# Performance work log

Hardware: AMD Instinct MI355X
Metric: run time of the kernel (lower is better)

## Reference

```python
import jax, jax.numpy as jnp
import numpy as np

B, S, C_IN, D, H = 16, 1024, 1280, 512, 8
HD = D // H  # head dim = 64
EPS = 1e-5


def _rope(x):
    # x: [b, h, s, d]; half-split rotation as in the torch module
    d = x.shape[-1]
    half = d // 2
    s = x.shape[2]
    inv_freq = 1.0 / (10000.0 ** (jnp.arange(0, d, 2, dtype=jnp.float32) / d))  # [half]
    ang = jnp.arange(s, dtype=jnp.float32)[:, None] * inv_freq[None, :]  # [s, half]
    sin, cos = jnp.sin(ang), jnp.cos(ang)  # broadcast over [b, h]
    x1, x2 = x[..., :half], x[..., half:]
    return jnp.concatenate([x1 * cos - x2 * sin, x1 * sin + x2 * cos], axis=-1)


def _ln(x, g, b):
    mu = jnp.mean(x, axis=-1, keepdims=True)
    var = jnp.mean((x - mu) ** 2, axis=-1, keepdims=True)
    return (x - mu) * jax.lax.rsqrt(var + EPS) * g + b


def setup_inputs() -> dict:
    key = jax.random.key(0)
    ks = jax.random.split(key, 12)
    def lin(k, fan_in, fan_out):
        lim = 1.0 / np.sqrt(fan_in)
        return jax.random.uniform(k, (fan_in, fan_out), jnp.float32, -lim, lim)
    return {
        "x": jax.random.normal(ks[0], (B, S, C_IN), jnp.float32),
        "w_in": lin(ks[1], C_IN, D), "b_in": jnp.zeros((D,), jnp.float32),
        "w_qkv": lin(ks[2], D, 3 * D), "b_qkv": jnp.zeros((3 * D,), jnp.float32),
        "w_out": lin(ks[3], D, D), "b_out": jnp.zeros((D,), jnp.float32),
        "w_ffn1": lin(ks[4], D, 4 * D), "b_ffn1": jnp.zeros((4 * D,), jnp.float32),
        "w_ffn2": lin(ks[5], 4 * D, D), "b_ffn2": jnp.zeros((D,), jnp.float32),
        "g1": jnp.ones((D,), jnp.float32), "bn1": jnp.zeros((D,), jnp.float32),
        "g2": jnp.ones((D,), jnp.float32), "bn2": jnp.zeros((D,), jnp.float32),
    }


def reference(x, w_in, b_in, w_qkv, b_qkv, w_out, b_out,
              w_ffn1, b_ffn1, w_ffn2, b_ffn2, g1, bn1, g2, bn2):
    h = x @ w_in + b_in  # [b, s, D]
    qkv = (h @ w_qkv + b_qkv).reshape(B, S, 3, H, HD)
    q, k, v = (jnp.transpose(qkv[:, :, i], (0, 2, 1, 3)) for i in range(3))  # [b, h, s, d]
    q, k = _rope(q), _rope(k)
    scores = jnp.einsum('bhqd,bhkd->bhqk', q, k) / np.sqrt(HD)
    attn = jax.nn.softmax(scores, axis=-1)
    o = jnp.einsum('bhqk,bhkd->bhqd', attn, v)
    o = jnp.transpose(o, (0, 2, 1, 3)).reshape(B, S, D)
    o = o @ w_out + b_out
    h = _ln(h + o, g1, bn1)
    ffn = jax.nn.relu(h @ w_ffn1 + b_ffn1) @ w_ffn2 + b_ffn2
    return _ln(h + ffn, g2, bn2)
```

## Files before the change

kernel.cpp:

```cpp
#include <hip/hip_runtime.h>
#include <hip/hip_bf16.h>
#include <math.h>

#define B_   16
#define S_   1024
#define CIN  1280
#define D_   512
#define H_   8
#define HD_  64
#define NROW (B_ * S_)

typedef __bf16 bf16;
typedef float  f32x2  __attribute__((ext_vector_type(2)));
typedef float  f32x4  __attribute__((ext_vector_type(4)));
typedef bf16   bf16x4 __attribute__((ext_vector_type(4)));
typedef bf16   bf16x8 __attribute__((ext_vector_type(8)));

__device__ __forceinline__ void gload_lds16(const bf16* g, bf16* l) {
    __builtin_amdgcn_global_load_lds(
        (const __attribute__((address_space(1))) void*)g,
        (__attribute__((address_space(3))) void*)l, 16, 0, 0);
}

#define SBAR()   __builtin_amdgcn_s_barrier()
#define SCHED0() __builtin_amdgcn_sched_barrier(0)
#define VMCNT8() asm volatile("s_waitcnt vmcnt(8)" ::: "memory")
#define VMCNT2() asm volatile("s_waitcnt vmcnt(2)" ::: "memory")
#define VMCNT0() asm volatile("s_waitcnt vmcnt(0)" ::: "memory")

__global__ void cvt_kernel(const float* __restrict__ in, bf16* __restrict__ out, int n4)
{
    int i = blockIdx.x * blockDim.x + threadIdx.x;
    if (i >= n4) return;
    f32x4 v = *(const f32x4*)(in + (size_t)i * 4);
    bf16x4 o;
    o[0] = (bf16)v[0]; o[1] = (bf16)v[1]; o[2] = (bf16)v[2]; o[3] = (bf16)v[3];
    *(bf16x4*)(out + (size_t)i * 4) = o;
}

__global__ __launch_bounds__(256)
void tr_cvt_kernel(const float* __restrict__ in, bf16* __restrict__ out, int R, int C)
{
    __shared__ float T[32][33];
    const int r0 = blockIdx.y << 5, c0 = blockIdx.x << 5;
    const int t  = threadIdx.x;
    {
        int lr = t >> 3, lc = (t & 7) << 2;
        f32x4 v = *(const f32x4*)(in + (size_t)(r0 + lr) * C + c0 + lc);
        T[lr][lc] = v[0]; T[lr][lc + 1] = v[1]; T[lr][lc + 2] = v[2]; T[lr][lc + 3] = v[3];
    }
    __syncthreads();
    {
        int oc = t >> 3, orr = (t & 7) << 2;
        bf16x4 o;
        o[0] = (bf16)T[orr][oc];     o[1] = (bf16)T[orr + 1][oc];
        o[2] = (bf16)T[orr + 2][oc]; o[3] = (bf16)T[orr + 3][oc];
        *(bf16x4*)(out + (size_t)(c0 + oc) * R + r0 + orr) = o;
    }
}

__global__ void cs_kernel(float* __restrict__ cs)
{
    int idx = blockIdx.x * 256 + threadIdx.x;
    int s = idx >> 5, i = idx & 31;
    float freq = exp2f(-(float)i * (13.287712379549449f / 32.f));
    float sn, c;
    sincosf((float)s * freq, &sn, &c);
    cs[(size_t)idx * 2]     = c;
    cs[(size_t)idx * 2 + 1] = sn;
}

#define ASZ1 (128 * 64)

template<int EPI, bool RELU, bool RES, bool OUTF, bool OUTB>
__global__ __launch_bounds__(256, 2)
void gemm128_kernel(const bf16* __restrict__ A, const bf16* __restrict__ Wt,
                    const float* __restrict__ bias, const bf16* __restrict__ res,
                    float* __restrict__ outf, bf16* __restrict__ outb,
                    const float* __restrict__ cs, bf16* __restrict__ vt,
                    int M, int N, int K)
{
    __shared__ bf16 lds[4 * ASZ1];

    const int tid  = threadIdx.x;
    const int lane = tid & 63;
    const int wid  = tid >> 6;

    const int perX = (M >> 7) >> 3;
    const int lin  = blockIdx.x;
    const int idx  = lin >> 3;
    const int my   = (lin & 7) * perX + (idx & (perX - 1));
    const int nx   = idx / perX;
    const int m0   = my << 7, n0 = nx << 7;

    const int sRow = lane >> 3;
    const int sK   = ((lane & 7) ^ sRow) << 3;

    const int r2  = wid >> 1;
    const int c2  = wid & 1;
    const int cc  = lane & 15;
    const int g   = (lane >> 4) & 3;
    const int swz = (cc & 7) << 4;

    f32x4 acc[4][4] = {};

    auto stage = [&](int t, int b) {
        const bf16* gA = A  + (size_t)m0 * K + t * 64;
        const bf16* gB = Wt + (size_t)n0 * K + t * 64;
        bf16* lA = lds + b * ASZ1;
        bf16* lB = lds + 2 * ASZ1 + b * ASZ1;
        #pragma unroll
        for (int v = 0; v < 4; ++v) {
            const int ch = v * 4 + wid;
            gload_lds16(gA + (size_t)(ch * 8 + sRow) * K + sK, lA + ch * 512);
            gload_lds16(gB + (size_t)(ch * 8 + sRow) * K + sK, lB + ch * 512);
        }
    };

    const int T = K >> 6;
    stage(0, 0);
    stage(1, 1);
    VMCNT8();
    SCHED0();
    SBAR();

    for (int t = 0; t < T; ++t) {
        const int b = t & 1;
        const char* lA = (const char*)(lds + b * ASZ1);
        const char* lB = (const char*)(lds + 2 * ASZ1 + b * ASZ1);

        #pragma unroll
        for (int ks = 0; ks < 2; ++ks) {
            bf16x8 af[4], bfr[4];
            #pragma unroll
            for (int i = 0; i < 4; ++i) {
                const int row = r2 * 64 + i * 16 + cc;
                af[i] = *(const bf16x8*)(lA + row * 128 + ((ks * 64 + g * 16) ^ swz));
            }
            #pragma unroll
            for (int j = 0; j < 4; ++j) {
                const int row = c2 * 64 + j * 16 + cc;
                bfr[j] = *(const bf16x8*)(lB + row * 128 + ((ks * 64 + g * 16) ^ swz));
            }
            __builtin_amdgcn_s_setprio(1);
            #pragma unroll
            for (int i = 0; i < 4; ++i)
                #pragma unroll
                for (int j = 0; j < 4; ++j)
                    acc[i][j] = __builtin_amdgcn_mfma_f32_16x16x32_bf16(af[i], bfr[j], acc[i][j], 0, 0, 0);
            __builtin_amdgcn_s_setprio(0);
        }
        SCHED0();
        SBAR();
        if (t + 2 < T) {
            stage(t + 2, b);
            VMCNT8();
        } else if (t + 1 < T) {
            VMCNT0();
        }
        if (t + 1 < T) { SCHED0(); SBAR(); }
    }

    const int rq = g << 2;
    if constexpr (EPI == 1) {
        const int colb = c2 * 64;
        if (nx < 8) {
            float bj[4];
            #pragma unroll
            for (int j = 0; j < 4; ++j) bj[j] = bias[n0 + colb + j * 16 + cc];
            #pragma unroll
            for (int i = 0; i < 4; ++i) {
                #pragma unroll
                for (int r = 0; r < 4; ++r) {
                    const int gm = m0 + r2 * 64 + i * 16 + rq + r;
                    const int s  = gm & (S_ - 1);
                    #pragma unroll
                    for (int jp = 0; jp < 2; ++jp) {
                        const int d = jp * 16 + cc;
                        f32x2 csv = *(const f32x2*)(cs + ((size_t)s * 32 + d) * 2);
                        float x1 = acc[i][jp][r]     + bj[jp];
                        float x2 = acc[i][jp + 2][r] + bj[jp + 2];
                        const size_t o1 = (size_t)gm * N + n0 + colb + d;
                        outb[o1]      = (bf16)(x1 * csv[0] - x2 * csv[1]);
                        outb[o1 + 32] = (bf16)(x1 * csv[1] + x2 * csv[0]);
                    }
                }
            }
        } else {
            const int col0 = n0 + colb;
            const int hw = (col0 >> 6) & 7;
            const int bb = m0 >> 10;
            bf16* vbase = vt + (size_t)(bb * 8 + hw) * (HD_ * S_);
            const int sb0 = (m0 & (S_ - 1)) + r2 * 64 + rq;
            #pragma unroll
            for (int i = 0; i < 4; ++i) {
                #pragma unroll
                for (int j = 0; j < 4; ++j) {
                    const int d = j * 16 + cc;
                    const float bv = bias[col0 + d];
                    bf16x4 pk;
                    #pragma unroll
                    for (int r = 0; r < 4; ++r) pk[r] = (bf16)(acc[i][j][r] + bv);
                    *(bf16x4*)(vbase + (size_t)d * S_ + sb0 + i * 16) = pk;
                }
            }
        }
    } else {
        #pragma unroll
        for (int i = 0; i < 4; ++i) {
            #pragma unroll
            for (int j = 0; j < 4; ++j) {
                const int gn = n0 + c2 * 64 + j * 16 + cc;
                const float bv = bias[gn];
                #pragma unroll
                for (int r = 0; r < 4; ++r) {
                    const int gm = m0 + r2 * 64 + i * 16 + rq + r;
                    float v = acc[i][j][r] + bv;
                    if (RES)  v += (float)res[(size_t)gm * N + gn];
                    if (RELU) v = fmaxf(v, 0.f);
                    if (OUTF) outf[(size_t)gm * N + gn] = v;
                    if (OUTB) outb[(size_t)gm * N + gn] = (bf16)v;
                }
            }
        }
    }
    (void)cs; (void)vt;
}

#define PST 72

__global__ __launch_bounds__(512)
void attn_kernel(const bf16* __restrict__ qkv, const bf16* __restrict__ vtg,
                 bf16* __restrict__ o)
{
    __shared__ bf16 Ks[2][4096];
    __shared__ bf16 Vs[2][4096];
    __shared__ bf16 Ps[8][16 * PST];

    const int bh  = blockIdx.x;
    const int b   = bh >> 3;
    const int h   = bh & 7;
    const int q0  = blockIdx.y << 7;
    const int tid = threadIdx.x;
    const int lane = tid & 63;
    const int w    = tid >> 6;
    const int c    = lane & 15;
    const int g    = lane >> 4;
    const int swz  = (c & 7) << 4;

    const size_t rs = 3 * D_;
    const bf16* qb = qkv + (size_t)b * S_ * rs + h * HD_;
    const bf16* kb = qb + D_;
    const bf16* vt = vtg + (size_t)bh * HD_ * S_;

    const int sRow = tid >> 3;
    const int sOff = ((tid & 7) ^ (sRow & 7)) << 3;

    bf16x8 qf[2];
    {
        const bf16* qrow = qb + (size_t)(q0 + w * 16 + c) * rs + g * 8;
        qf[0] = *(const bf16x8*)(qrow);
        qf[1] = *(const bf16x8*)(qrow + 32);
    }
    SCHED0();

    bf16x8 vones;
    {
        bf16 one = (bf16)(c == 0 ? 1.f : 0.f);
        #pragma unroll
        for (int u = 0; u < 8; ++u) vones[u] = one;
    }

    auto stage = [&](int t, int buf) {
        gload_lds16(kb + (size_t)(t * 64 + sRow) * rs + sOff, &Ks[buf][0] + (size_t)tid * 8);
        gload_lds16(vt + (size_t)sRow * S_ + t * 64 + sOff,   &Vs[buf][0] + (size_t)tid * 8);
    };

    f32x4 oa[4] = {};
    f32x4 oa5 = {};
    float m_r = -3.0e38f;
    const float CE  = 0.18033688011112042f;
    const float THR = 44.3614195558365f;

    stage(0, 0);
    stage(1, 1);
    VMCNT2();
    SCHED0();
    SBAR();

    for (int t = 0; t < 16; ++t) {
        const int buf = t & 1;
        const char* kB = (const char*)Ks[buf];
        const char* vB = (const char*)Vs[buf];

        f32x4 sa[4] = {};
        __builtin_amdgcn_s_setprio(1);
        #pragma unroll
        for (int ch = 0; ch < 2; ++ch)
            #pragma unroll
            for (int ks = 0; ks < 4; ++ks) {
                bf16x8 kf = *(const bf16x8*)(kB + (ks * 16 + c) * 128 + ((ch * 64 + g * 16) ^ swz));
                sa[ks] = __builtin_amdgcn_mfma_f32_16x16x32_bf16(kf, qf[ch], sa[ks], 0, 0, 0);
            }
        __builtin_amdgcn_s_setprio(0);

        float pmax = -3.0e38f;
        #pragma unroll
        for (int ks = 0; ks < 4; ++ks)
            pmax = fmaxf(pmax, fmaxf(fmaxf(sa[ks][0], sa[ks][1]), fmaxf(sa[ks][2], sa[ks][3])));
        pmax = fmaxf(pmax, __shfl_xor(pmax, 16, 64));
        pmax = fmaxf(pmax, __shfl_xor(pmax, 32, 64));

        if (!__all(pmax - m_r <= THR)) {
            float mnew = fmaxf(m_r, pmax);
            float sc = __builtin_amdgcn_exp2f((m_r - mnew) * CE);
            #pragma unroll
            for (int r = 0; r < 4; ++r) {
                float scr = __shfl(sc, g * 4 + r, 64);
                #pragma unroll
                for (int j = 0; j < 4; ++j) oa[j][r] *= scr;
                oa5[r] *= scr;
            }
            m_r = mnew;
        }

        const float nmCE = -m_r * CE;
        #pragma unroll
        for (int ks = 0; ks < 4; ++ks) {
            bf16x4 pb;
            #pragma unroll
            for (int r = 0; r < 4; ++r)
                pb[r] = (bf16)__builtin_amdgcn_exp2f(__builtin_fmaf(sa[ks][r], CE, nmCE));
            *(bf16x4*)&Ps[w][c * PST + ks * 16 + g * 4] = pb;
        }

        __builtin_amdgcn_s_setprio(1);
        #pragma unroll
        for (int ch = 0; ch < 2; ++ch) {
            bf16x8 pa = *(const bf16x8*)&Ps[w][c * PST + ch * 32 + g * 8];
            #pragma unroll
            for (int j = 0; j < 4; ++j) {
                bf16x8 vf = *(const bf16x8*)(vB + (j * 16 + c) * 128 + ((ch * 64 + g * 16) ^ swz));
                oa[j] = __builtin_amdgcn_mfma_f32_16x16x32_bf16(pa, vf, oa[j], 0, 0, 0);
            }
            oa5 = __builtin_amdgcn_mfma_f32_16x16x32_bf16(pa, vones, oa5, 0, 0, 0);
        }
        __builtin_amdgcn_s_setprio(0);

        SCHED0();
        SBAR();
        if (t + 2 < 16) {
            stage(t + 2, buf);
            VMCNT2();
        } else if (t + 1 < 16) {
            VMCNT0();
        }
        if (t + 1 < 16) { SCHED0(); SBAR(); }
    }

    float linv[4];
    #pragma unroll
    for (int r = 0; r < 4; ++r)
        linv[r] = 1.f / __shfl(oa5[r], lane & 48, 64);
    #pragma unroll
    for (int j = 0; j < 4; ++j)
        #pragma unroll
        for (int r = 0; r < 4; ++r) {
            int q = q0 + w * 16 + g * 4 + r;
            o[((size_t)(b * S_) + q) * D_ + h * HD_ + j * 16 + c] = (bf16)(oa[j][r] * linv[r]);
        }
}

template<bool OUTF, bool OUTB>
__global__ __launch_bounds__(256)
void ln_kernel(const float* __restrict__ in, const float* __restrict__ g,
               const float* __restrict__ be, float* __restrict__ outf,
               bf16* __restrict__ outb)
{
    const int row  = (blockIdx.x << 2) + (threadIdx.x >> 6);
    const int lane = threadIdx.x & 63;
    const float* p = in + (size_t)row * D_;
    f32x4 a  = *(const f32x4*)(p + lane * 4);
    f32x4 b2 = *(const f32x4*)(p + 256 + lane * 4);
    float s  = a[0] + a[1] + a[2] + a[3] + b2[0] + b2[1] + b2[2] + b2[3];
    float s2 = a[0]*a[0] + a[1]*a[1] + a[2]*a[2] + a[3]*a[3]
             + b2[0]*b2[0] + b2[1]*b2[1] + b2[2]*b2[2] + b2[3]*b2[3];
    #pragma unroll
    for (int off = 32; off; off >>= 1) {
        s  += __shfl_xor(s,  off, 64);
        s2 += __shfl_xor(s2, off, 64);
    }
    const float mean = s * (1.f / 512.f);
    const float var  = s2 * (1.f / 512.f) - mean * mean;
    const float rstd = rsqrtf(var + 1e-5f);

    f32x4 g0 = *(const f32x4*)(g + lane * 4);
    f32x4 g1 = *(const f32x4*)(g + 256 + lane * 4);
    f32x4 e0 = *(const f32x4*)(be + lane * 4);
    f32x4 e1 = *(const f32x4*)(be + 256 + lane * 4);
    f32x4 o0, o1;
    #pragma unroll
    for (int u = 0; u < 4; u++) {
        o0[u] = (a[u]  - mean) * rstd * g0[u] + e0[u];
        o1[u] = (b2[u] - mean) * rstd * g1[u] + e1[u];
    }
    if (OUTF) {
        float* of = outf + (size_t)row * D_;
        *(f32x4*)(of + lane * 4)       = o0;
        *(f32x4*)(of + 256 + lane * 4) = o1;
    }
    if (OUTB) {
        bf16x4 c0, c1;
        #pragma unroll
        for (int u = 0; u < 4; u++) { c0[u] = (bf16)o0[u]; c1[u] = (bf16)o1[u]; }
        bf16* ob = outb + (size_t)row * D_;
        *(bf16x4*)(ob + lane * 4)       = c0;
        *(bf16x4*)(ob + 256 + lane * 4) = c1;
    }
}

extern "C" void kernel_launch(void* const* d_in, const int* in_sizes, int n_in,
                              void* d_out, int out_size, void* d_ws, size_t ws_size,
                              hipStream_t stream)
{
    const float* x      = (const float*)d_in[0];
    const float* w_in   = (const float*)d_in[1];
    const float* b_in   = (const float*)d_in[2];
    const float* w_qkv  = (const float*)d_in[3];
    const float* b_qkv  = (const float*)d_in[4];
    const float* w_out  = (const float*)d_in[5];
    const float* b_out  = (const float*)d_in[6];
    const float* w_ffn1 = (const float*)d_in[7];
    const float* b_ffn1 = (const float*)d_in[8];
    const float* w_ffn2 = (const float*)d_in[9];
    const float* b_ffn2 = (const float*)d_in[10];
    const float* g1     = (const float*)d_in[11];
    const float* bn1    = (const float*)d_in[12];
    const float* g2     = (const float*)d_in[13];
    const float* bn2    = (const float*)d_in[14];

    char* ws = (char*)d_ws;
    constexpr size_t OFF_XB   = 0;
    constexpr size_t OFF_WIN  = OFF_XB   + 41943040ull;
    constexpr size_t OFF_WQKV = OFF_WIN  + 1310720ull;
    constexpr size_t OFF_WOUT = OFF_WQKV + 1572864ull;
    constexpr size_t OFF_WF1  = OFF_WOUT + 524288ull;
    constexpr size_t OFF_WF2  = OFF_WF1  + 2097152ull;
    constexpr size_t OFF_CS   = OFF_WF2  + 2097152ull;
    constexpr size_t OFF_HB   = OFF_CS   + 33554432ull;
    constexpr size_t OFF_QKV  = OFF_HB   + 16777216ull;
    constexpr size_t OFF_OB   = OFF_QKV  + 50331648ull;
    constexpr size_t OFF_VT   = OFF_OB   + 16777216ull;
    constexpr size_t OFF_H2B  = OFF_VT   + 33554432ull;
    constexpr size_t OFF_F1   = OFF_H2B  + 16777216ull;
    constexpr size_t OFF_T1   = OFF_XB;
    constexpr size_t OFF_T2   = OFF_QKV;

    bf16*  x_b    = (bf16*)(ws + OFF_XB);
    bf16*  win_t  = (bf16*)(ws + OFF_WIN);
    bf16*  wqkv_t = (bf16*)(ws + OFF_WQKV);
    bf16*  wout_t = (bf16*)(ws + OFF_WOUT);
    bf16*  wf1_t  = (bf16*)(ws + OFF_WF1);
    bf16*  wf2_t  = (bf16*)(ws + OFF_WF2);
    float* cs_t   = (float*)(ws + OFF_CS);
    bf16*  h_b    = (bf16*)(ws + OFF_HB);
    bf16*  qkv_b  = (bf16*)(ws + OFF_QKV);
    bf16*  o_b    = (bf16*)(ws + OFF_OB);
    bf16*  vt_g   = (bf16*)(ws + OFF_VT);
    bf16*  h2_b   = (bf16*)(ws + OFF_H2B);
    bf16*  f1_b   = (bf16*)(ws + OFF_F1);
    float* t1_f   = (float*)(ws + OFF_T1);
    float* t2_f   = (float*)(ws + OFF_T2);

    {
        int n4 = NROW * CIN / 4;
        cvt_kernel<<<(n4 + 255) / 256, 256, 0, stream>>>(x, x_b, n4);
    }
    tr_cvt_kernel<<<dim3(512/32, 1280/32), 256, 0, stream>>>(w_in,   win_t,  1280, 512);
    tr_cvt_kernel<<<dim3(1536/32, 512/32), 256, 0, stream>>>(w_qkv,  wqkv_t, 512, 1536);
    tr_cvt_kernel<<<dim3(512/32,  512/32), 256, 0, stream>>>(w_out,  wout_t, 512, 512);
    tr_cvt_kernel<<<dim3(2048/32, 512/32), 256, 0, stream>>>(w_ffn1, wf1_t,  512, 2048);
    tr_cvt_kernel<<<dim3(512/32, 2048/32), 256, 0, stream>>>(w_ffn2, wf2_t,  2048, 512);
    cs_kernel<<<128, 256, 0, stream>>>(cs_t);

    gemm128_kernel<0,false,false,false,true><<<(NROW/128) * (D_/128), 256, 0, stream>>>(
        x_b, win_t, b_in, nullptr, nullptr, h_b, nullptr, nullptr, NROW, D_, CIN);
    gemm128_kernel<1,false,false,false,true><<<(NROW/128) * (3*D_/128), 256, 0, stream>>>(
        h_b, wqkv_t, b_qkv, nullptr, nullptr, qkv_b, cs_t, vt_g, NROW, 3*D_, D_);
    attn_kernel<<<dim3(B_*H_, S_/128), 512, 0, stream>>>(qkv_b, vt_g, o_b);
    gemm128_kernel<0,false,true,true,false><<<(NROW/128) * (D_/128), 256, 0, stream>>>(
        o_b, wout_t, b_out, h_b, t1_f, nullptr, nullptr, nullptr, NROW, D_, D_);
    ln_kernel<false,true><<<NROW/4, 256, 0, stream>>>(t1_f, g1, bn1, nullptr, h2_b);
    gemm128_kernel<0,true,false,false,true><<<(NROW/128) * (4*D_/128), 256, 0, stream>>>(
        h2_b, wf1_t, b_ffn1, nullptr, nullptr, f1_b, nullptr, nullptr, NROW, 4*D_, D_);
    gemm128_kernel<0,false,true,true,false><<<(NROW/128) * (D_/128), 256, 0, stream>>>(
        f1_b, wf2_t, b_ffn2, h2_b, t2_f, nullptr, nullptr, nullptr, NROW, D_, 4*D_);
    ln_kernel<true,false><<<NROW/4, 256, 0, stream>>>(t2_f, g2, bn2, (float*)d_out, nullptr);

    (void)in_sizes; (void)n_in; (void)out_size; (void)ws_size;
}
```

Baseline: 275.7 us.

## Fuse prep kernels into one launch and double query rows per attention block

Merges the input conversion, five weight transpose-conversions and the RoPE table kernel into a single prep kernel that dispatches on block index, cutting six launches. The attention kernel now has each wave process two 16-row query sub-tiles (256 queries per block), so every K/V tile staged in LDS is reused by twice as many MFMAs and the grid is halved. In exchange it raises register pressure and the P scratch buffer in LDS, and halves the number of attention blocks, which lowers parallelism.

New measurement: 265.1 us. -3.8%, faster.

```diff
diff --git a/kernel.cpp b/kernel.cpp
--- a/kernel.cpp
+++ b/kernel.cpp
@@ -28,22 +28,12 @@
 #define VMCNT2() asm volatile("s_waitcnt vmcnt(2)" ::: "memory")
 #define VMCNT0() asm volatile("s_waitcnt vmcnt(0)" ::: "memory")
 
-__global__ void cvt_kernel(const float* __restrict__ in, bf16* __restrict__ out, int n4)
-{
-    int i = blockIdx.x * blockDim.x + threadIdx.x;
-    if (i >= n4) return;
-    f32x4 v = *(const f32x4*)(in + (size_t)i * 4);
-    bf16x4 o;
-    o[0] = (bf16)v[0]; o[1] = (bf16)v[1]; o[2] = (bf16)v[2]; o[3] = (bf16)v[3];
-    *(bf16x4*)(out + (size_t)i * 4) = o;
-}
-
-__global__ __launch_bounds__(256)
-void tr_cvt_kernel(const float* __restrict__ in, bf16* __restrict__ out, int R, int C)
+__device__ __forceinline__ void tr_tile(const float* __restrict__ in,
+                                        bf16* __restrict__ out,
+                                        int R, int C, int cx, int ry, int t)
 {
     __shared__ float T[32][33];
-    const int r0 = blockIdx.y << 5, c0 = blockIdx.x << 5;
-    const int t  = threadIdx.x;
+    const int r0 = ry << 5, c0 = cx << 5;
     {
         int lr = t >> 3, lc = (t & 7) << 2;
         f32x4 v = *(const f32x4*)(in + (size_t)(r0 + lr) * C + c0 + lc);
@@ -59,16 +49,49 @@
     }
 }
 
-__global__ void cs_kernel(float* __restrict__ cs)
+#define NCVT (NROW * CIN / 4 / 256)
+
+__global__ __launch_bounds__(256)
+void prep_kernel(const float* __restrict__ x, bf16* __restrict__ x_b,
+                 const float* __restrict__ w_in,   bf16* __restrict__ win_t,
+                 const float* __restrict__ w_qkv,  bf16* __restrict__ wqkv_t,
+                 const float* __restrict__ w_out,  bf16* __restrict__ wout_t,
+                 const float* __restrict__ w_ffn1, bf16* __restrict__ wf1_t,
+                 const float* __restrict__ w_ffn2, bf16* __restrict__ wf2_t,
+                 float* __restrict__ cs)
 {
-    int idx = blockIdx.x * 256 + threadIdx.x;
-    int s = idx >> 5, i = idx & 31;
-    float freq = exp2f(-(float)i * (13.287712379549449f / 32.f));
-    float sn, c;
-    sincosf((float)s * freq, &sn, &c);
-    cs[(size_t)idx * 2]     = c;
-    cs[(size_t)idx * 2 + 1] = sn;
-}
+    const int t   = threadIdx.x;
+    int bid = blockIdx.x;
+    if (bid < NCVT) {
+        int i = bid * 256 + t;
+        f32x4 v = *(const f32x4*)(x + (size_t)i * 4);
+        bf16x4 o;
+        o[0] = (bf16)v[0]; o[1] = (bf16)v[1]; o[2] = (bf16)v[2]; o[3] = (bf16)v[3];
+        *(bf16x4*)(x_b + (size_t)i * 4) = o;
+        return;
+    }
+    bid -= NCVT;
+    if (bid < 640)  { tr_tile(w_in,   win_t,  1280, 512,  bid % 16, bid / 16, t); return; }
+    bid -= 640;
+    if (bid < 768)  { tr_tile(w_qkv,  wqkv_t, 512,  1536, bid % 48, bid / 48, t); return; }
+    bid -= 768;
+    if (bid < 256)  { tr_tile(w_out,  wout_t, 512,  512,  bid % 16, bid / 16, t); return; }
+    bid -= 256;
+    if (bid < 1024) { tr_tile(w_ffn1, wf1_t,  512,  2048, bid % 64, bid / 64, t); return; }
+    bid -= 1024;
+    if (bid < 1024) { tr_tile(w_ffn2, wf2_t,  2048, 512,  bid % 16, bid / 16, t); return; }
+    bid -= 1024;
+    {
+        int idx = bid * 256 + t;
+        int s = idx >> 5, i = idx & 31;
+        float freq = exp2f(-(float)i * (13.287712379549449f / 32.f));
+        float sn, c;
+        sincosf((float)s * freq, &sn, &c);
+        cs[(size_t)idx * 2]     = c;
+        cs[(size_t)idx * 2 + 1] = sn;
+    }
+}
+#define NPREP (NCVT + 640 + 768 + 256 + 1024 + 1024 + 128)
 
 #define ASZ1 (128 * 64)
 
@@ -235,12 +258,12 @@
 {
     __shared__ bf16 Ks[2][4096];
     __shared__ bf16 Vs[2][4096];
-    __shared__ bf16 Ps[8][16 * PST];
+    __shared__ bf16 Ps[16][16 * PST];
 
     const int bh  = blockIdx.x;
     const int b   = bh >> 3;
     const int h   = bh & 7;
-    const int q0  = blockIdx.y << 7;
+    const int q0  = blockIdx.y << 8;
     const int tid = threadIdx.x;
     const int lane = tid & 63;
     const int w    = tid >> 6;
@@ -256,11 +279,12 @@
     const int sRow = tid >> 3;
     const int sOff = ((tid & 7) ^ (sRow & 7)) << 3;
 
-    bf16x8 qf[2];
-    {
-        const bf16* qrow = qb + (size_t)(q0 + w * 16 + c) * rs + g * 8;
-        qf[0] = *(const bf16x8*)(qrow);
-        qf[1] = *(const bf16x8*)(qrow + 32);
+    bf16x8 qf[2][2];
+    #pragma unroll
+    for (int s = 0; s < 2; ++s) {
+        const bf16* qrow = qb + (size_t)(q0 + s * 128 + w * 16 + c) * rs + g * 8;
+        qf[s][0] = *(const bf16x8*)(qrow);
+        qf[s][1] = *(const bf16x8*)(qrow + 32);
     }
     SCHED0();
 
@@ -276,9 +300,9 @@
         gload_lds16(vt + (size_t)sRow * S_ + t * 64 + sOff,   &Vs[buf][0] + (size_t)tid * 8);
     };
 
-    f32x4 oa[4] = {};
-    f32x4 oa5 = {};
-    float m_r = -3.0e38f;
+    f32x4 oa[2][4] = {};
+    f32x4 oa5[2] = {};
+    float m_r[2] = {-3.0e38f, -3.0e38f};
     const float CE  = 0.18033688011112042f;
     const float THR = 44.3614195558365f;
 
@@ -293,57 +317,65 @@
         const char* kB = (const char*)Ks[buf];
         const char* vB = (const char*)Vs[buf];
 
-        f32x4 sa[4] = {};
+        f32x4 sa[2][4] = {};
         __builtin_amdgcn_s_setprio(1);
         #pragma unroll
         for (int ch = 0; ch < 2; ++ch)
             #pragma unroll
             for (int ks = 0; ks < 4; ++ks) {
                 bf16x8 kf = *(const bf16x8*)(kB + (ks * 16 + c) * 128 + ((ch * 64 + g * 16) ^ swz));
-                sa[ks] = __builtin_amdgcn_mfma_f32_16x16x32_bf16(kf, qf[ch], sa[ks], 0, 0, 0);
+                sa[0][ks] = __builtin_amdgcn_mfma_f32_16x16x32_bf16(kf, qf[0][ch], sa[0][ks], 0, 0, 0);
+                sa[1][ks] = __builtin_amdgcn_mfma_f32_16x16x32_bf16(kf, qf[1][ch], sa[1][ks], 0, 0, 0);
             }
         __builtin_amdgcn_s_setprio(0);
 
-        float pmax = -3.0e38f;
-        #pragma unroll
-        for (int ks = 0; ks < 4; ++ks)
-            pmax = fmaxf(pmax, fmaxf(fmaxf(sa[ks][0], sa[ks][1]), fmaxf(sa[ks][2], sa[ks][3])));
-        pmax = fmaxf(pmax, __shfl_xor(pmax, 16, 64));
-        pmax = fmaxf(pmax, __shfl_xor(pmax, 32, 64));
-
-        if (!__all(pmax - m_r <= THR)) {
-            float mnew = fmaxf(m_r, pmax);
-            float sc = __builtin_amdgcn_exp2f((m_r - mnew) * CE);
-            #pragma unroll
-            for (int r = 0; r < 4; ++r) {
-                float scr = __shfl(sc, g * 4 + r, 64);
+        #pragma unroll
+        for (int s = 0; s < 2; ++s) {
+            float pmax = -3.0e38f;
+            #pragma unroll
+            for (int ks = 0; ks < 4; ++ks)
+                pmax = fmaxf(pmax, fmaxf(fmaxf(sa[s][ks][0], sa[s][ks][1]),
+                                         fmaxf(sa[s][ks][2], sa[s][ks][3])));
+            pmax = fmaxf(pmax, __shfl_xor(pmax, 16, 64));
+            pmax = fmaxf(pmax, __shfl_xor(pmax, 32, 64));
+
+            if (!__all(pmax - m_r[s] <= THR)) {
+                float mnew = fmaxf(m_r[s], pmax);
+                float sc = __builtin_amdgcn_exp2f((m_r[s] - mnew) * CE);
                 #pragma unroll
-                for (int j = 0; j < 4; ++j) oa[j][r] *= scr;
-                oa5[r] *= scr;
-            }
-            m_r = mnew;
-        }
-
-        const float nmCE = -m_r * CE;
-        #pragma unroll
-        for (int ks = 0; ks < 4; ++ks) {
-            bf16x4 pb;
-            #pragma unroll
-            for (int r = 0; r < 4; ++r)
-                pb[r] = (bf16)__builtin_amdgcn_exp2f(__builtin_fmaf(sa[ks][r], CE, nmCE));
-            *(bf16x4*)&Ps[w][c * PST + ks * 16 + g * 4] = pb;
+                for (int r = 0; r < 4; ++r) {
+                    float scr = __shfl(sc, g * 4 + r, 64);
+                    #pragma unroll
+                    for (int j = 0; j < 4; ++j) oa[s][j][r] *= scr;
+                    oa5[s][r] *= scr;
+                }
+                m_r[s] = mnew;
+            }
+
+            const float nmCE = -m_r[s] * CE;
+            #pragma unroll
+            for (int ks = 0; ks < 4; ++ks) {
+                bf16x4 pb;
+                #pragma unroll
+                for (int r = 0; r < 4; ++r)
+                    pb[r] = (bf16)__builtin_amdgcn_exp2f(__builtin_fmaf(sa[s][ks][r], CE, nmCE));
+                *(bf16x4*)&Ps[w * 2 + s][c * PST + ks * 16 + g * 4] = pb;
+            }
         }
 
         __builtin_amdgcn_s_setprio(1);
         #pragma unroll
         for (int ch = 0; ch < 2; ++ch) {
-            bf16x8 pa = *(const bf16x8*)&Ps[w][c * PST + ch * 32 + g * 8];
+            bf16x8 pa0 = *(const bf16x8*)&Ps[w * 2 + 0][c * PST + ch * 32 + g * 8];
+            bf16x8 pa1 = *(const bf16x8*)&Ps[w * 2 + 1][c * PST + ch * 32 + g * 8];
             #pragma unroll
             for (int j = 0; j < 4; ++j) {
                 bf16x8 vf = *(const bf16x8*)(vB + (j * 16 + c) * 128 + ((ch * 64 + g * 16) ^ swz));
-                oa[j] = __builtin_amdgcn_mfma_f32_16x16x32_bf16(pa, vf, oa[j], 0, 0, 0);
-            }
-            oa5 = __builtin_amdgcn_mfma_f32_16x16x32_bf16(pa, vones, oa5, 0, 0, 0);
+                oa[0][j] = __builtin_amdgcn_mfma_f32_16x16x32_bf16(pa0, vf, oa[0][j], 0, 0, 0);
+                oa[1][j] = __builtin_amdgcn_mfma_f32_16x16x32_bf16(pa1, vf, oa[1][j], 0, 0, 0);
+            }
+            oa5[0] = __builtin_amdgcn_mfma_f32_16x16x32_bf16(pa0, vones, oa5[0], 0, 0, 0);
+            oa5[1] = __builtin_amdgcn_mfma_f32_16x16x32_bf16(pa1, vones, oa5[1], 0, 0, 0);
         }
         __builtin_amdgcn_s_setprio(0);
 
@@ -358,17 +390,20 @@
         if (t + 1 < 16) { SCHED0(); SBAR(); }
     }
 
-    float linv[4];
     #pragma unroll
-    for (int r = 0; r < 4; ++r)
-        linv[r] = 1.f / __shfl(oa5[r], lane & 48, 64);
-    #pragma unroll
-    for (int j = 0; j < 4; ++j)
-        #pragma unroll
-        for (int r = 0; r < 4; ++r) {
-            int q = q0 + w * 16 + g * 4 + r;
-            o[((size_t)(b * S_) + q) * D_ + h * HD_ + j * 16 + c] = (bf16)(oa[j][r] * linv[r]);
-        }
+    for (int s = 0; s < 2; ++s) {
+        float linv[4];
+        #pragma unroll
+        for (int r = 0; r < 4; ++r)
+            linv[r] = 1.f / __shfl(oa5[s][r], lane & 48, 64);
+        #pragma unroll
+        for (int j = 0; j < 4; ++j)
+            #pragma unroll
+            for (int r = 0; r < 4; ++r) {
+                int q = q0 + s * 128 + w * 16 + g * 4 + r;
+                o[((size_t)(b * S_) + q) * D_ + h * HD_ + j * 16 + c] = (bf16)(oa[s][j][r] * linv[r]);
+            }
+    }
 }
 
 template<bool OUTF, bool OUTB>
@@ -472,22 +507,15 @@
     float* t1_f   = (float*)(ws + OFF_T1);
     float* t2_f   = (float*)(ws + OFF_T2);
 
-    {
-        int n4 = NROW * CIN / 4;
-        cvt_kernel<<<(n4 + 255) / 256, 256, 0, stream>>>(x, x_b, n4);
-    }
-    tr_cvt_kernel<<<dim3(512/32, 1280/32), 256, 0, stream>>>(w_in,   win_t,  1280, 512);
-    tr_cvt_kernel<<<dim3(1536/32, 512/32), 256, 0, stream>>>(w_qkv,  wqkv_t, 512, 1536);
-    tr_cvt_kernel<<<dim3(512/32,  512/32), 256, 0, stream>>>(w_out,  wout_t, 512, 512);
-    tr_cvt_kernel<<<dim3(2048/32, 512/32), 256, 0, stream>>>(w_ffn1, wf1_t,  512, 2048);
-    tr_cvt_kernel<<<dim3(512/32, 2048/32), 256, 0, stream>>>(w_ffn2, wf2_t,  2048, 512);
-    cs_kernel<<<128, 256, 0, stream>>>(cs_t);
+    prep_kernel<<<NPREP, 256, 0, stream>>>(x, x_b, w_in, win_t, w_qkv, wqkv_t,
+                                           w_out, wout_t, w_ffn1, wf1_t,
+                                           w_ffn2, wf2_t, cs_t);
 
     gemm128_kernel<0,false,false,false,true><<<(NROW/128) * (D_/128), 256, 0, stream>>>(
         x_b, win_t, b_in, nullptr, nullptr, h_b, nullptr, nullptr, NROW, D_, CIN);
     gemm128_kernel<1,false,false,false,true><<<(NROW/128) * (3*D_/128), 256, 0, stream>>>(
         h_b, wqkv_t, b_qkv, nullptr, nullptr, qkv_b, cs_t, vt_g, NROW, 3*D_, D_);
-    attn_kernel<<<dim3(B_*H_, S_/128), 512, 0, stream>>>(qkv_b, vt_g, o_b);
+    attn_kernel<<<dim3(B_*H_, S_/256), 512, 0, stream>>>(qkv_b, vt_g, o_b);
     gemm128_kernel<0,false,true,true,false><<<(NROW/128) * (D_/128), 256, 0, stream>>>(
         o_b, wout_t, b_out, h_b, t1_f, nullptr, nullptr, nullptr, NROW, D_, D_);
     ln_kernel<false,true><<<NROW/4, 256, 0, stream>>>(t1_f, g1, bn1, nullptr, h2_b);
```
